# Kernel tuning notes

Measured on AMD Instinct MI355X. Metric: run time of the kernel, lower is better.

## Reference

```python
import jax, jax.numpy as jnp
import numpy as np

N = 50000
E = 1600000
EPS = 1e-16


def transformer_conv(x, src, dst, ea, Wq, bq, Wk, bk, Wv, bv, We, Ws, bs):
    # PyG TransformerConv, heads=1, concat=True, root_weight=True
    C = Wq.shape[1]
    q = x @ Wq + bq                      # [N, C]
    k = x @ Wk + bk                      # [N, C]
    v = x @ Wv + bv                      # [N, C]
    e = ea @ We                          # [E, C]
    k_e = k[src] + e                     # per-edge key
    v_e = v[src] + e                     # per-edge value
    score = (q[dst] * k_e).sum(-1) / jnp.sqrt(jnp.asarray(C, x.dtype))  # [E]
    # segment softmax over incoming edges of each dst node
    m = jax.ops.segment_max(score, dst, num_segments=N)
    ex = jnp.exp(score - m[dst])
    denom = jax.ops.segment_sum(ex, dst, num_segments=N)
    alpha = ex / (denom[dst] + EPS)
    out = jax.ops.segment_sum(alpha[:, None] * v_e, dst, num_segments=N)
    return out + x @ Ws + bs             # skip connection


def gcn_conv(x, src, dst, W, b):
    # PyG GCNConv: self-loops + symmetric deg^-1/2 normalization
    n_idx = jnp.arange(N)
    src2 = jnp.concatenate([src, n_idx])
    dst2 = jnp.concatenate([dst, n_idx])
    deg = jax.ops.segment_sum(jnp.ones(E + N, x.dtype), dst2, num_segments=N)
    dinv = jnp.where(deg > 0, jax.lax.rsqrt(deg), 0.0)
    norm = dinv[src2] * dinv[dst2]       # [E+N]
    h = x @ W                            # [N, out]
    out = jax.ops.segment_sum(norm[:, None] * h[src2], dst2, num_segments=N)
    return out + b


def setup_inputs() -> dict:
    key = jax.random.key(0)
    ks = jax.random.split(key, 32)
    d = {}
    d['x'] = jax.random.normal(ks[0], (N, 128), jnp.float32)
    d['edge_index'] = jax.random.randint(ks[1], (2, E), 0, N, jnp.int64)
    d['edge_attr'] = jax.random.normal(ks[2], (E, 16), jnp.float32)
    shapes = dict(
        Wq1=(128, 96), bq1=(96,), Wk1=(128, 96), bk1=(96,), Wv1=(128, 96), bv1=(96,),
        We1=(16, 96), Ws1=(128, 96), bs1=(96,),
        Wq2=(96, 64), bq2=(64,), Wk2=(96, 64), bk2=(64,), Wv2=(96, 64), bv2=(64,),
        We2=(16, 64), Ws2=(96, 64), bs2=(64,),
        Wmu=(64, 32), bmu=(32,), Wls=(64, 32), bls=(32,))
    for i, (name, shp) in enumerate(shapes.items()):
        scale = 1.0 / np.sqrt(shp[0]) if len(shp) == 2 else 0.02
        d[name] = jax.random.normal(ks[3 + i], shp, jnp.float32) * scale
    return d


def reference(x, edge_index, edge_attr,
              Wq1, bq1, Wk1, bk1, Wv1, bv1, We1, Ws1, bs1,
              Wq2, bq2, Wk2, bk2, Wv2, bv2, We2, Ws2, bs2,
              Wmu, bmu, Wls, bls):
    src, dst = edge_index[0], edge_index[1]
    h = jax.nn.relu(transformer_conv(x, src, dst, edge_attr,
                                     Wq1, bq1, Wk1, bk1, Wv1, bv1, We1, Ws1, bs1))
    h = jax.nn.relu(transformer_conv(h, src, dst, edge_attr,
                                     Wq2, bq2, Wk2, bk2, Wv2, bv2, We2, Ws2, bs2))
    mu = gcn_conv(h, src, dst, Wmu, bmu)
    logstd = gcn_conv(h, src, dst, Wls, bls)
    return mu, logstd
```

## Files before the change

### kernel.cpp

```cpp
#include <hip/hip_runtime.h>
#include <math.h>


#define TPB 256
typedef unsigned int uint32;
typedef unsigned short u16;
typedef __attribute__((ext_vector_type(4))) float f32x4;
typedef __attribute__((ext_vector_type(4))) uint32 u32x4;
typedef __attribute__((ext_vector_type(8))) short bf16x8;

__device__ __forceinline__ uint32 f2bf(float f) {
    uint32 u = __float_as_uint(f);
    return (u + 0x7fffu + ((u >> 16) & 1u)) >> 16;
}
__device__ __forceinline__ float bf2f(uint32 b) { return __uint_as_float(b << 16); }

__global__ void hist_kernel(const int* __restrict__ dst, int* __restrict__ deg, int E) {
    int i = blockIdx.x * TPB + threadIdx.x;
    if (i < E) atomicAdd(&deg[__builtin_nontemporal_load(dst + i)], 1);
}

__global__ __launch_bounds__(1024) void scan1_kernel(const int* __restrict__ deg,
                                                     int* __restrict__ prowp,
                                                     int* __restrict__ bsum, int n) {
    __shared__ int wsum[16];
    __shared__ int woff[16];
    int tid = threadIdx.x;
    int i = blockIdx.x * 1024 + tid;
    int lane = tid & 63, w = tid >> 6;
    int dg = (i < n) ? deg[i] : 0;
    int x = (dg + 7) & ~7;
    int v = x;
#pragma unroll
    for (int off = 1; off < 64; off <<= 1) {
        int t = __shfl_up(v, off, 64);
        if (lane >= off) v += t;
    }
    if (lane == 63) wsum[w] = v;
    __syncthreads();
    if (tid < 64) {
        int s = (tid < 16) ? wsum[tid] : 0;
#pragma unroll
        for (int off = 1; off < 16; off <<= 1) {
            int t = __shfl_up(s, off, 64);
            if (lane >= off) s += t;
        }
        if (tid < 16) woff[tid] = s;
    }
    __syncthreads();
    int incl = v + (w ? woff[w - 1] : 0);
    if (i < n) prowp[i] = incl;
    if (tid == 1023) bsum[blockIdx.x] = incl;
}

__global__ void scan2_kernel(const int* __restrict__ bsum, int* __restrict__ boff,
                             int* __restrict__ prowpN, int nb) {
    int tid = threadIdx.x;
    int x = (tid < nb) ? bsum[tid] : 0;
    int v = x;
#pragma unroll
    for (int off = 1; off < 64; off <<= 1) {
        int t = __shfl_up(v, off, 64);
        if (tid >= off) v += t;
    }
    if (tid < nb) boff[tid] = v - x;
    if (tid == nb - 1) *prowpN = v;
}

__global__ __launch_bounds__(1024) void scan3_kernel(const int* __restrict__ deg,
                                                     const int* __restrict__ boff,
                                                     int* __restrict__ prowp,
                                                     int* __restrict__ cursor,
                                                     float* __restrict__ dinv, int n) {
    int i = blockIdx.x * 1024 + threadIdx.x;
    if (i < n) {
        int dg = deg[i];
        int x = (dg + 7) & ~7;
        int excl = prowp[i] - x + boff[blockIdx.x];
        prowp[i] = excl;
        cursor[i] = excl;
        dinv[i] = 1.0f / sqrtf((float)(dg + 1));
    }
}

__global__ void scatter_kernel(const int* __restrict__ src, const int* __restrict__ dst,
                               const float* __restrict__ EA,
                               int* __restrict__ cursor,
                               int* __restrict__ psrc, u16* __restrict__ EAb, int E) {
    int i = blockIdx.x * TPB + threadIdx.x;
    if (i >= E) return;
    int pos = atomicAdd(&cursor[__builtin_nontemporal_load(dst + i)], 1);
    psrc[pos] = __builtin_nontemporal_load(src + i);
    const f32x4* e4 = (const f32x4*)(EA + (size_t)i * 16);
    f32x4 a = __builtin_nontemporal_load(e4);
    f32x4 b = __builtin_nontemporal_load(e4 + 1);
    f32x4 c = __builtin_nontemporal_load(e4 + 2);
    f32x4 d = __builtin_nontemporal_load(e4 + 3);
    u32x4* o = (u32x4*)(EAb + (size_t)pos * 16);
    u32x4 lo = {f2bf(a.x) | (f2bf(a.y) << 16), f2bf(a.z) | (f2bf(a.w) << 16),
                f2bf(b.x) | (f2bf(b.y) << 16), f2bf(b.z) | (f2bf(b.w) << 16)};
    u32x4 hi = {f2bf(c.x) | (f2bf(c.y) << 16), f2bf(c.z) | (f2bf(c.w) << 16),
                f2bf(d.x) | (f2bf(d.y) << 16), f2bf(d.z) | (f2bf(d.w) << 16)};
    o[0] = lo;
    o[1] = hi;
}

__global__ void padfill_kernel(const int* __restrict__ prowp, const int* __restrict__ deg,
                               int* __restrict__ psrc, u16* __restrict__ EAb, int N) {
    int n = blockIdx.x * TPB + threadIdx.x;
    if (n >= N) return;
    int p = prowp[n] + deg[n], pe = prowp[n + 1];
    u32x4 z = {0u, 0u, 0u, 0u};
    for (; p < pe; ++p) {
        psrc[p] = N;
        u32x4* o = (u32x4*)(EAb + (size_t)p * 16);
        o[0] = z;
        o[1] = z;
    }
}

__global__ void pack_kernel(
    const float* Wq1, const float* Wk1, const float* Wv1, const float* Ws1,
    const float* bq1, const float* bk1, const float* bv1, const float* bs1,
    const float* We1,
    const float* Wq2, const float* Wk2, const float* Wv2, const float* Ws2,
    const float* bq2, const float* bk2, const float* bv2, const float* bs2,
    const float* We2,
    const float* Wmu, const float* bmu, const float* Wls, const float* bls,
    const float* x, unsigned short* xb, int NX,
    unsigned short* Wc1t, float* bc1, unsigned short* Wc2t, float* bc2,
    float* Wc3, float* bc3) {
    const float s1 = 0.1020620726159658f;
    const float s2 = 0.125f;
    int gi = blockIdx.x * TPB + threadIdx.x;
    const int R0 = 448 * 128, R1 = R0 + 320 * 96, R2 = R1 + 64 * 64;
    const int R3 = R2 + 448, R4 = R3 + 320, R5 = R4 + 64;
    for (int i = gi; i < R5; i += gridDim.x * TPB) {
        if (i < R0) {
            int c = i / 128, kk = i % 128;
            float v = 0.f;
            if (c < 96) v = Wq1[kk * 96 + c] * s1;
            else if (c < 112) {
                int t = c - 96; float a = 0.f;
                for (int u = 0; u < 96; ++u) a += Wq1[kk * 96 + u] * We1[t * 96 + u];
                v = a * s1;
            } else if (c < 304) {
                int tt = c - 112;
                v = (tt & 1) ? Wv1[kk * 96 + (tt >> 1)] : Wk1[kk * 96 + (tt >> 1)];
            } else if (c < 400) v = Ws1[kk * 96 + (c - 304)];
            Wc1t[i] = (unsigned short)f2bf(v);
        } else if (i < R1) {
            int j = i - R0;
            int c = j / 96, kk = j % 96;
            float v = 0.f;
            if (c < 64) v = Wq2[kk * 64 + c] * s2;
            else if (c < 80) {
                int t = c - 64; float a = 0.f;
                for (int u = 0; u < 64; ++u) a += Wq2[kk * 64 + u] * We2[t * 64 + u];
                v = a * s2;
            } else if (c < 208) {
                int tt = c - 80;
                v = (tt & 1) ? Wv2[kk * 64 + (tt >> 1)] : Wk2[kk * 64 + (tt >> 1)];
            } else if (c < 272) v = Ws2[kk * 64 + (c - 208)];
            Wc2t[j] = (unsigned short)f2bf(v);
        } else if (i < R2) {
            int j = i - R1;
            int k = j / 64, c = j % 64;
            Wc3[j] = (c < 32) ? Wmu[k * 32 + c] : Wls[k * 32 + (c - 32)];
        } else if (i < R3) {
            int c = i - R2;
            float v = 0.f;
            if (c < 96) v = bq1[c] * s1;
            else if (c < 112) {
                int t = c - 96; float a = 0.f;
                for (int u = 0; u < 96; ++u) a += bq1[u] * We1[t * 96 + u];
                v = a * s1;
            } else if (c < 304) {
                int tt = c - 112;
                v = (tt & 1) ? bv1[tt >> 1] : bk1[tt >> 1];
            } else if (c < 400) v = bs1[c - 304];
            bc1[c] = v;
        } else if (i < R4) {
            int c = i - R3;
            float v = 0.f;
            if (c < 64) v = bq2[c] * s2;
            else if (c < 80) {
                int t = c - 64; float a = 0.f;
                for (int u = 0; u < 64; ++u) a += bq2[u] * We2[t * 64 + u];
                v = a * s2;
            } else if (c < 208) {
                int tt = c - 80;
                v = (tt & 1) ? bv2[tt >> 1] : bk2[tt >> 1];
            } else if (c < 272) v = bs2[c - 208];
            bc2[c] = v;
        } else {
            int c = i - R4;
            bc3[c] = (c < 32) ? bmu[c] : bls[c - 32];
        }
    }
    for (int i = gi; i < NX; i += gridDim.x * TPB)
        xb[i] = (unsigned short)f2bf(x[i]);
}

__global__ __launch_bounds__(256) void mfma_gemm_kernel(
    const unsigned short* __restrict__ A,
    const unsigned short* __restrict__ Wt,
    const float* __restrict__ bias,
    float* __restrict__ Qs, float* __restrict__ QE,
    uint32* __restrict__ KVp, float* __restrict__ SK,
    int N, int K, int Cq) {
    __shared__ unsigned short As[64][56];
    __shared__ unsigned short Bs[64][56];
    int r0 = blockIdx.x * 64, c0 = blockIdx.y * 64;
    int tid = threadIdx.x;
    int lane = tid & 63, w = tid >> 6;
    int wm = w >> 1, wn = w & 1;
    int l15 = lane & 15, l4 = lane >> 4;
    f32x4 zero = {0.f, 0.f, 0.f, 0.f};
    f32x4 acc[2][2] = {{zero, zero}, {zero, zero}};
    int sr = tid >> 2, sk = (tid & 3) * 8;

    for (int kc = 0; kc < K; kc += 32) {
        bf16x8 av = {};
        int ar = r0 + sr;
        if (ar < N) av = *(const bf16x8*)(A + (size_t)ar * K + kc + sk);
        *(bf16x8*)&As[sr][sk] = av;
        bf16x8 bv = *(const bf16x8*)(Wt + (size_t)(c0 + sr) * K + kc + sk);
        *(bf16x8*)&Bs[sr][sk] = bv;
        __syncthreads();
        bf16x8 af0 = *(const bf16x8*)&As[32 * wm + l15][l4 * 8];
        bf16x8 af1 = *(const bf16x8*)&As[32 * wm + 16 + l15][l4 * 8];
        bf16x8 bf0 = *(const bf16x8*)&Bs[32 * wn + l15][l4 * 8];
        bf16x8 bf1 = *(const bf16x8*)&Bs[32 * wn + 16 + l15][l4 * 8];
        acc[0][0] = __builtin_amdgcn_mfma_f32_16x16x32_bf16(af0, bf0, acc[0][0], 0, 0, 0);
        acc[0][1] = __builtin_amdgcn_mfma_f32_16x16x32_bf16(af0, bf1, acc[0][1], 0, 0, 0);
        acc[1][0] = __builtin_amdgcn_mfma_f32_16x16x32_bf16(af1, bf0, acc[1][0], 0, 0, 0);
        acc[1][1] = __builtin_amdgcn_mfma_f32_16x16x32_bf16(af1, bf1, acc[1][1], 0, 0, 0);
        __syncthreads();
    }

    int qe0 = Cq, kv0 = Cq + 16, sk0 = 3 * Cq + 16, end0 = 4 * Cq + 16;
#pragma unroll
    for (int fm = 0; fm < 2; ++fm) {
#pragma unroll
        for (int fn = 0; fn < 2; ++fn) {
            int cb = c0 + 32 * wn + 16 * fn;
            int c = cb + l15;
            float bia = bias[c];
#pragma unroll
            for (int r = 0; r < 4; ++r) {
                int row = r0 + 32 * wm + 16 * fm + l4 * 4 + r;
                float v = acc[fm][fn][r] + bia;
                float pv = __shfl_xor(v, 1, 64);
                bool ok = row < N;
                if (cb < qe0) {
                    if (ok) Qs[(size_t)row * Cq + c] = v;
                } else if (cb < kv0) {
                    if (ok) QE[(size_t)row * 16 + (c - qe0)] = v;
                } else if (cb < sk0) {
                    if (ok && !(l15 & 1)) {
                        int t = c - kv0;
                        KVp[(size_t)row * Cq + (t >> 1)] = (f2bf(v) << 16) | f2bf(pv);
                    }
                } else if (cb < end0) {
                    if (ok) SK[(size_t)row * Cq + (c - sk0)] = v;
                }
            }
        }
    }
}

template <int C>
__global__ __launch_bounds__(256) void edge_attn_kernel(
    const float* __restrict__ Qs, const float* __restrict__ SK,
    const uint32* __restrict__ KVp,
    const u16* __restrict__ EAb, const float* __restrict__ QE,
    const int* __restrict__ prowp, const int* __restrict__ deg,
    const int* __restrict__ psrc,
    float* __restrict__ Hpre, float* __restrict__ AEA, int N) {
    constexpr int CPL = C / 32;
    int n = blockIdx.x * 4 + (threadIdx.x >> 6);
    if (n >= N) return;
    int lane = threadIdx.x & 63;
    int half = lane >> 5, l = lane & 31, t16 = l & 15;
    bool lo16 = (l < 16);

    uint32 nC = (uint32)n * C;
    float q[CPL], acc[CPL];
#pragma unroll
    for (int j = 0; j < CPL; ++j) { q[j] = Qs[nC + l + 32 * j]; acc[j] = 0.f; }
    float qe = lo16 ? QE[(uint32)n * 16 + t16] : 0.f;
    float d = 0.f, aea = 0.f;
    int eb = prowp[n], ee = prowp[n + 1];

    for (int base = eb + 8 * half; base < ee; base += 16) {
        const int* sp = psrc + base;
        const u16* ep = EAb + (size_t)base * 16 + t16;
        float dots[8], eav[8];
        uint32 kv[8][CPL];
#pragma unroll
        for (int u = 0; u < 8; ++u) {
            int s = __builtin_nontemporal_load(sp + u);
            eav[u] = bf2f(__builtin_nontemporal_load(ep + u * 16));
            uint32 off = (uint32)s * C + l;
            float dt = qe * eav[u];
#pragma unroll
            for (int j = 0; j < CPL; ++j) {
                uint32 t = KVp[off + 32 * j];
                kv[u][j] = t;
                dt = fmaf(q[j], __uint_as_float(t & 0xffff0000u), dt);
            }
            dots[u] = dt;
        }
#pragma unroll
        for (int a = 0; a < 4; ++a) {
            float x0 = dots[2 * a], x1 = dots[2 * a + 1];
            float z = (lo16 ? x0 : x1) + __shfl_xor(lo16 ? x1 : x0, 16, 64);
            z += __shfl_xor(z, 8, 64);
            z += __shfl_xor(z, 4, 64);
            z += __shfl_xor(z, 2, 64);
            z += __shfl_xor(z, 1, 64);
            float p = __expf(z);
            float p0 = __shfl(p, 0, 32);
            float p1 = __shfl(p, 16, 32);
            d += p0 + p1;
            aea = fmaf(p0, eav[2 * a], fmaf(p1, eav[2 * a + 1], aea));
#pragma unroll
            for (int j = 0; j < CPL; ++j)
                acc[j] = fmaf(p0, __uint_as_float(kv[2 * a][j] << 16),
                         fmaf(p1, __uint_as_float(kv[2 * a + 1][j] << 16), acc[j]));
        }
    }
    d += __shfl_xor(d, 32, 64);
    aea += __shfl_xor(aea, 32, 64);
    d -= (float)((ee - eb) - deg[n]);
    float inv = 1.f / (d + 1e-16f);
#pragma unroll
    for (int j = 0; j < CPL; ++j) {
        float a2 = acc[j] + __shfl_xor(acc[j], 32, 64);
        if (half == 0)
            Hpre[nC + l + 32 * j] = a2 * inv + SK[nC + l + 32 * j];
    }
    if (lane < 16) AEA[(uint32)n * 16 + t16] = aea * inv;
}

template <int C>
__global__ void fixup_relu_kernel(const float* __restrict__ Hpre, const float* __restrict__ AEA,
                                  const float* __restrict__ We,
                                  unsigned short* __restrict__ H1b, int NC) {
    int idx = blockIdx.x * TPB + threadIdx.x;
    if (idx >= NC) return;
    int n = idx / C, c = idx % C;
    const float* a = AEA + (size_t)n * 16;
    float s = Hpre[idx];
#pragma unroll
    for (int t = 0; t < 16; ++t) s += a[t] * We[t * C + c];
    H1b[idx] = (unsigned short)f2bf(fmaxf(s, 0.f));
}

__global__ void fixup2_kernel(const float* __restrict__ Hpre, const float* __restrict__ AEA,
                              const float* __restrict__ We, const float* __restrict__ dinv,
                              uint32* __restrict__ H2p, int N) {
    int idx = blockIdx.x * TPB + threadIdx.x;
    if (idx >= N * 32) return;
    int n = idx >> 5, c = idx & 31;
    const float* a = AEA + (size_t)n * 16;
    float s0 = Hpre[(size_t)n * 64 + c];
    float s1 = Hpre[(size_t)n * 64 + 32 + c];
#pragma unroll
    for (int t = 0; t < 16; ++t) {
        s0 += a[t] * We[t * 64 + c];
        s1 += a[t] * We[t * 64 + 32 + c];
    }
    float dn = dinv[n];
    s0 = fmaxf(s0, 0.f) * dn;
    s1 = fmaxf(s1, 0.f) * dn;
    H2p[idx] = f2bf(s0) | (f2bf(s1) << 16);
}

__global__ __launch_bounds__(256) void gcn_agg_kernel(
    const uint32* __restrict__ H2p, const int* __restrict__ prowp,
    const int* __restrict__ psrc, const float* __restrict__ dinv,
    float* __restrict__ AGG, int N) {
    int n = blockIdx.x * 4 + (threadIdx.x >> 6);
    if (n >= N) return;
    int lane = threadIdx.x & 63, half = lane >> 5, l = lane & 31;
    float s0 = 0.f, s1 = 0.f;
    int eb = prowp[n], ee = prowp[n + 1];
    for (int base = eb + 8 * half; base < ee; base += 16) {
        const int* sp = psrc + base;
#pragma unroll
        for (int u = 0; u < 8; ++u) {
            int s = __builtin_nontemporal_load(sp + u);
            uint32 t = H2p[(uint32)s * 32 + l];
            s0 += bf2f(t & 0xffffu);
            s1 += __uint_as_float(t & 0xffff0000u);
        }
    }
    s0 += __shfl_xor(s0, 32, 64);
    s1 += __shfl_xor(s1, 32, 64);
    if (half == 0) {
        uint32 u = H2p[(uint32)n * 32 + l];
        float dn = dinv[n];
        AGG[(uint32)n * 64 + l]      = dn * (s0 + bf2f(u & 0xffffu));
        AGG[(uint32)n * 64 + 32 + l] = dn * (s1 + __uint_as_float(u & 0xffff0000u));
    }
}

template <int CT, bool SPLIT>
__global__ __launch_bounds__(256) void gemm_kernel(
    const float* __restrict__ A, const float* __restrict__ W,
    const float* __restrict__ bias, float* __restrict__ Out,
    float* __restrict__ Out2, int N, int K, int C) {
    constexpr int TC = CT / 16;
    __shared__ float As[32][68];
    __shared__ float Bs[32][CT + 4];
    int r0 = blockIdx.x * 64, c0 = blockIdx.y * CT;
    int t = threadIdx.x;
    int tr = t >> 4, tc = t & 15;
    float acc[4][TC];
#pragma unroll
    for (int i = 0; i < 4; ++i)
#pragma unroll
        for (int j = 0; j < TC; ++j) acc[i][j] = 0.f;

    for (int kc = 0; kc < K; kc += 32) {
        int ra = t >> 2, kq = (t & 3) * 8;
        float4 a0 = {0, 0, 0, 0}, a1 = {0, 0, 0, 0};
        int r = r0 + ra;
        if (r < N) {
            const float* ap = A + (size_t)r * K + kc + kq;
            a0 = *(const float4*)ap;
            a1 = *(const float4*)(ap + 4);
        }
        As[kq + 0][ra] = a0.x; As[kq + 1][ra] = a0.y;
        As[kq + 2][ra] = a0.z; As[kq + 3][ra] = a0.w;
        As[kq + 4][ra] = a1.x; As[kq + 5][ra] = a1.y;
        As[kq + 6][ra] = a1.z; As[kq + 7][ra] = a1.w;
        constexpr int PASSES = (32 * CT) / (256 * 8);
#pragma unroll
        for (int p = 0; p < PASSES; ++p) {
            int idx = (t + p * 256) * 8;
            int k = idx / CT, c = idx % CT;
            const float* wp = W + (size_t)(kc + k) * C + c0 + c;
            float4 b0 = *(const float4*)wp;
            float4 b1 = *(const float4*)(wp + 4);
            *(float4*)&Bs[k][c] = b0;
            *(float4*)&Bs[k][c + 4] = b1;
        }
        __syncthreads();
#pragma unroll
        for (int k = 0; k < 32; ++k) {
            float4 av = *(const float4*)&As[k][tr * 4];
            float a[4] = {av.x, av.y, av.z, av.w};
#pragma unroll
            for (int u = 0; u < TC / 4; ++u) {
                float4 bv = *(const float4*)&Bs[k][tc * TC + u * 4];
                float b[4] = {bv.x, bv.y, bv.z, bv.w};
#pragma unroll
                for (int i = 0; i < 4; ++i)
#pragma unroll
                    for (int j = 0; j < 4; ++j) acc[i][u * 4 + j] += a[i] * b[j];
            }
        }
        __syncthreads();
    }
#pragma unroll
    for (int i = 0; i < 4; ++i) {
        int r = r0 + tr * 4 + i;
        if (r >= N) continue;
#pragma unroll
        for (int j = 0; j < TC; ++j) {
            int c = c0 + tc * TC + j;
            float v = acc[i][j] + bias[c];
            if (SPLIT) {
                if (c < 32) Out[(size_t)r * 32 + c] = v;
                else        Out2[(size_t)r * 32 + c - 32] = v;
            } else {
                Out[(size_t)r * C + c] = v;
            }
        }
    }
}

extern "C" void kernel_launch(void* const* d_in, const int* in_sizes, int n_in,
                              void* d_out, int out_size, void* d_ws, size_t ws_size,
                              hipStream_t stream) {
    const float* x   = (const float*)d_in[0];
    const int*   ei  = (const int*)d_in[1];
    const float* ea  = (const float*)d_in[2];
    const float* Wq1 = (const float*)d_in[3];  const float* bq1 = (const float*)d_in[4];
    const float* Wk1 = (const float*)d_in[5];  const float* bk1 = (const float*)d_in[6];
    const float* Wv1 = (const float*)d_in[7];  const float* bv1 = (const float*)d_in[8];
    const float* We1 = (const float*)d_in[9];
    const float* Ws1 = (const float*)d_in[10]; const float* bs1 = (const float*)d_in[11];
    const float* Wq2 = (const float*)d_in[12]; const float* bq2 = (const float*)d_in[13];
    const float* Wk2 = (const float*)d_in[14]; const float* bk2 = (const float*)d_in[15];
    const float* Wv2 = (const float*)d_in[16]; const float* bv2 = (const float*)d_in[17];
    const float* We2 = (const float*)d_in[18];
    const float* Ws2 = (const float*)d_in[19]; const float* bs2 = (const float*)d_in[20];
    const float* Wmu = (const float*)d_in[21]; const float* bmu = (const float*)d_in[22];
    const float* Wls = (const float*)d_in[23]; const float* bls = (const float*)d_in[24];

    int N = in_sizes[0] / 128;
    int E = in_sizes[1] / 2;
    const int* src = ei;
    const int* dst = ei + E;
    int E2max = E + 8 * N;

    char* ws = (char*)d_ws;
    size_t off = 0;
    auto alloc = [&](size_t bytes) -> char* {
        char* p = ws + off;
        off = (off + bytes + 255) & ~(size_t)255;
        return p;
    };
    int*      deg    = (int*)alloc((size_t)N * 4);
    int*      prowp  = (int*)alloc((size_t)(N + 1) * 4);
    int*      cursor = (int*)alloc((size_t)N * 4);
    float*    dinv   = (float*)alloc((size_t)N * 4);
    int*      bsum   = (int*)alloc(256 * 4);
    int*      boff   = (int*)alloc(256 * 4);
    int*      psrc   = (int*)alloc((size_t)E2max * 4);
    u16*      EAb    = (u16*)alloc((size_t)E2max * 16 * 2);
    unsigned short* Wc1t = (unsigned short*)alloc(448 * 128 * 2);
    float*    bc1    = (float*)alloc(448 * 4);
    unsigned short* Wc2t = (unsigned short*)alloc(320 * 96 * 2);
    float*    bc2    = (float*)alloc(320 * 4);
    float*    Wc3    = (float*)alloc(64 * 64 * 4);
    float*    bc3    = (float*)alloc(64 * 4);
    unsigned short* xb = (unsigned short*)alloc((size_t)N * 128 * 2);
    float*    Qs   = (float*)alloc((size_t)N * 96 * 4);
    float*    QE   = (float*)alloc((size_t)N * 16 * 4);
    uint32*   KVp  = (uint32*)alloc((size_t)(N + 1) * 96 * 4);
    float*    SKb  = (float*)alloc((size_t)N * 96 * 4);
    float*    Hpre = (float*)alloc((size_t)N * 96 * 4);
    unsigned short* H1b = (unsigned short*)alloc((size_t)N * 96 * 2);
    float*    AEA  = (float*)alloc((size_t)N * 16 * 4);
    uint32*   H2p  = (uint32*)alloc((size_t)(N + 1) * 32 * 4);
    float*    AGG  = (float*)alloc((size_t)N * 64 * 4);

    (void)hipMemsetAsync(deg, 0, (size_t)N * 4, stream);
    (void)hipMemsetAsync(KVp + (size_t)N * 96, 0, 96 * 4, stream);
    (void)hipMemsetAsync(H2p + (size_t)N * 32, 0, 32 * 4, stream);

    int ebk = (E + TPB - 1) / TPB;
    int nb1k = (N + 1023) / 1024;
    int nbN = (N + TPB - 1) / TPB;
    hist_kernel<<<ebk, TPB, 0, stream>>>(dst, deg, E);
    scan1_kernel<<<nb1k, 1024, 0, stream>>>(deg, prowp, bsum, N);
    scan2_kernel<<<1, 64, 0, stream>>>(bsum, boff, prowp + N, nb1k);
    scan3_kernel<<<nb1k, 1024, 0, stream>>>(deg, boff, prowp, cursor, dinv, N);
    scatter_kernel<<<ebk, TPB, 0, stream>>>(src, dst, ea, cursor, psrc, EAb, E);
    padfill_kernel<<<nbN, TPB, 0, stream>>>(prowp, deg, psrc, EAb, N);
    pack_kernel<<<364, TPB, 0, stream>>>(Wq1, Wk1, Wv1, Ws1, bq1, bk1, bv1, bs1, We1,
                                         Wq2, Wk2, Wv2, Ws2, bq2, bk2, bv2, bs2, We2,
                                         Wmu, bmu, Wls, bls, x, xb, N * 128,
                                         Wc1t, bc1, Wc2t, bc2, Wc3, bc3);

    int rb = (N + 63) / 64;
    int nb4 = (N + 3) / 4;

    mfma_gemm_kernel<<<dim3(rb, 7), 256, 0, stream>>>(xb, Wc1t, bc1, Qs, QE, KVp, SKb,
                                                      N, 128, 96);
    edge_attn_kernel<96><<<nb4, 256, 0, stream>>>(Qs, SKb, KVp, EAb, QE, prowp, deg, psrc,
                                                  Hpre, AEA, N);
    fixup_relu_kernel<96><<<(N * 96 + TPB - 1) / TPB, TPB, 0, stream>>>(Hpre, AEA, We1,
                                                                        H1b, N * 96);
    mfma_gemm_kernel<<<dim3(rb, 5), 256, 0, stream>>>(H1b, Wc2t, bc2, Qs, QE, KVp, SKb,
                                                      N, 96, 64);
    (void)hipMemsetAsync(KVp + (size_t)N * 64, 0, 64 * 4, stream);
    edge_attn_kernel<64><<<nb4, 256, 0, stream>>>(Qs, SKb, KVp, EAb, QE, prowp, deg, psrc,
                                                  Hpre, AEA, N);
    fixup2_kernel<<<(N * 32 + TPB - 1) / TPB, TPB, 0, stream>>>(Hpre, AEA, We2, dinv, H2p, N);
    gcn_agg_kernel<<<nb4, 256, 0, stream>>>(H2p, prowp, psrc, dinv, AGG, N);
    gemm_kernel<64, true><<<dim3(rb, 1), 256, 0, stream>>>(AGG, Wc3, bc3, (float*)d_out,
                                                           (float*)d_out + (size_t)N * 32,
                                                           N, 64, 64);
}
```

Baseline: 518.6 us.

## Store edge attributes in original order and index them via packed edge IDs

The scatter kernel now writes bf16 edge attributes sequentially by original edge index with nontemporal stores, instead of scattering 32-byte rows to CSR positions. The CSR array becomes a packed 64-bit (edge id, source) pair, and padding points at a zero row appended after the last edge. This makes the scatter pass write coalesced, but the edge-attention kernels now gather edge-attribute rows randomly through the edge id, and the CSR array read by three kernels doubles in size.

```diff
diff --git a/kernel.cpp b/kernel.cpp
--- a/kernel.cpp
+++ b/kernel.cpp
@@ -4,6 +4,7 @@
 
 #define TPB 256
 typedef unsigned int uint32;
+typedef unsigned long long u64;
 typedef unsigned short u16;
 typedef __attribute__((ext_vector_type(4))) float f32x4;
 typedef __attribute__((ext_vector_type(4))) uint32 u32x4;
@@ -86,37 +87,38 @@
 __global__ void scatter_kernel(const int* __restrict__ src, const int* __restrict__ dst,
                                const float* __restrict__ EA,
                                int* __restrict__ cursor,
-                               int* __restrict__ psrc, u16* __restrict__ EAb, int E) {
+                               u64* __restrict__ pse, u16* __restrict__ EAbE, int E) {
     int i = blockIdx.x * TPB + threadIdx.x;
     if (i >= E) return;
-    int pos = atomicAdd(&cursor[__builtin_nontemporal_load(dst + i)], 1);
-    psrc[pos] = __builtin_nontemporal_load(src + i);
+    int s = __builtin_nontemporal_load(src + i);
+    int d0 = __builtin_nontemporal_load(dst + i);
+    int pos = atomicAdd(&cursor[d0], 1);
+    pse[pos] = ((u64)(uint32)i << 32) | (uint32)s;
     const f32x4* e4 = (const f32x4*)(EA + (size_t)i * 16);
     f32x4 a = __builtin_nontemporal_load(e4);
     f32x4 b = __builtin_nontemporal_load(e4 + 1);
     f32x4 c = __builtin_nontemporal_load(e4 + 2);
     f32x4 d = __builtin_nontemporal_load(e4 + 3);
-    u32x4* o = (u32x4*)(EAb + (size_t)pos * 16);
     u32x4 lo = {f2bf(a.x) | (f2bf(a.y) << 16), f2bf(a.z) | (f2bf(a.w) << 16),
                 f2bf(b.x) | (f2bf(b.y) << 16), f2bf(b.z) | (f2bf(b.w) << 16)};
     u32x4 hi = {f2bf(c.x) | (f2bf(c.y) << 16), f2bf(c.z) | (f2bf(c.w) << 16),
                 f2bf(d.x) | (f2bf(d.y) << 16), f2bf(d.z) | (f2bf(d.w) << 16)};
-    o[0] = lo;
-    o[1] = hi;
+    u32x4* o = (u32x4*)(EAbE + (size_t)i * 16);
+    __builtin_nontemporal_store(lo, o);
+    __builtin_nontemporal_store(hi, o + 1);
 }
 
 __global__ void padfill_kernel(const int* __restrict__ prowp, const int* __restrict__ deg,
-                               int* __restrict__ psrc, u16* __restrict__ EAb, int N) {
+                               u64* __restrict__ pse, int N, int E) {
     int n = blockIdx.x * TPB + threadIdx.x;
     if (n >= N) return;
     int p = prowp[n] + deg[n], pe = prowp[n + 1];
-    u32x4 z = {0u, 0u, 0u, 0u};
-    for (; p < pe; ++p) {
-        psrc[p] = N;
-        u32x4* o = (u32x4*)(EAb + (size_t)p * 16);
-        o[0] = z;
-        o[1] = z;
-    }
+    u64 pad = ((u64)(uint32)E << 32) | (uint32)N;
+    for (; p < pe; ++p) pse[p] = pad;
+}
+
+__global__ void zerorow_kernel(u16* __restrict__ EAbE, int E) {
+    if (threadIdx.x < 16) EAbE[(size_t)E * 16 + threadIdx.x] = 0;
 }
 
 __global__ void pack_kernel(
@@ -274,9 +276,9 @@
 __global__ __launch_bounds__(256) void edge_attn_kernel(
     const float* __restrict__ Qs, const float* __restrict__ SK,
     const uint32* __restrict__ KVp,
-    const u16* __restrict__ EAb, const float* __restrict__ QE,
+    const u16* __restrict__ EAbE, const float* __restrict__ QE,
     const int* __restrict__ prowp, const int* __restrict__ deg,
-    const int* __restrict__ psrc,
+    const u64* __restrict__ pse,
     float* __restrict__ Hpre, float* __restrict__ AEA, int N) {
     constexpr int CPL = C / 32;
     int n = blockIdx.x * 4 + (threadIdx.x >> 6);
@@ -294,15 +296,16 @@
     int eb = prowp[n], ee = prowp[n + 1];
 
     for (int base = eb + 8 * half; base < ee; base += 16) {
-        const int* sp = psrc + base;
-        const u16* ep = EAb + (size_t)base * 16 + t16;
+        const u64* pp = pse + base;
         float dots[8], eav[8];
         uint32 kv[8][CPL];
 #pragma unroll
         for (int u = 0; u < 8; ++u) {
-            int s = __builtin_nontemporal_load(sp + u);
-            eav[u] = bf2f(__builtin_nontemporal_load(ep + u * 16));
-            uint32 off = (uint32)s * C + l;
+            u64 pk = __builtin_nontemporal_load(pp + u);
+            uint32 s = (uint32)pk;
+            uint32 eid = (uint32)(pk >> 32);
+            eav[u] = bf2f((uint32)EAbE[(size_t)eid * 16 + t16]);
+            uint32 off = s * C + l;
             float dt = qe * eav[u];
 #pragma unroll
             for (int j = 0; j < CPL; ++j) {
@@ -380,7 +383,7 @@
 
 __global__ __launch_bounds__(256) void gcn_agg_kernel(
     const uint32* __restrict__ H2p, const int* __restrict__ prowp,
-    const int* __restrict__ psrc, const float* __restrict__ dinv,
+    const u64* __restrict__ pse, const float* __restrict__ dinv,
     float* __restrict__ AGG, int N) {
     int n = blockIdx.x * 4 + (threadIdx.x >> 6);
     if (n >= N) return;
@@ -388,11 +391,11 @@
     float s0 = 0.f, s1 = 0.f;
     int eb = prowp[n], ee = prowp[n + 1];
     for (int base = eb + 8 * half; base < ee; base += 16) {
-        const int* sp = psrc + base;
+        const u64* pp = pse + base;
 #pragma unroll
         for (int u = 0; u < 8; ++u) {
-            int s = __builtin_nontemporal_load(sp + u);
-            uint32 t = H2p[(uint32)s * 32 + l];
+            uint32 s = (uint32)__builtin_nontemporal_load(pp + u);
+            uint32 t = H2p[s * 32 + l];
             s0 += bf2f(t & 0xffffu);
             s1 += __uint_as_float(t & 0xffff0000u);
         }
@@ -521,8 +524,8 @@
     float*    dinv   = (float*)alloc((size_t)N * 4);
     int*      bsum   = (int*)alloc(256 * 4);
     int*      boff   = (int*)alloc(256 * 4);
-    int*      psrc   = (int*)alloc((size_t)E2max * 4);
-    u16*      EAb    = (u16*)alloc((size_t)E2max * 16 * 2);
+    u64*      pse    = (u64*)alloc((size_t)E2max * 8);
+    u16*      EAbE   = (u16*)alloc((size_t)(E + 1) * 16 * 2);
     unsigned short* Wc1t = (unsigned short*)alloc(448 * 128 * 2);
     float*    bc1    = (float*)alloc(448 * 4);
     unsigned short* Wc2t = (unsigned short*)alloc(320 * 96 * 2);
@@ -551,8 +554,9 @@
     scan1_kernel<<<nb1k, 1024, 0, stream>>>(deg, prowp, bsum, N);
     scan2_kernel<<<1, 64, 0, stream>>>(bsum, boff, prowp + N, nb1k);
     scan3_kernel<<<nb1k, 1024, 0, stream>>>(deg, boff, prowp, cursor, dinv, N);
-    scatter_kernel<<<ebk, TPB, 0, stream>>>(src, dst, ea, cursor, psrc, EAb, E);
-    padfill_kernel<<<nbN, TPB, 0, stream>>>(prowp, deg, psrc, EAb, N);
+    scatter_kernel<<<ebk, TPB, 0, stream>>>(src, dst, ea, cursor, pse, EAbE, E);
+    padfill_kernel<<<nbN, TPB, 0, stream>>>(prowp, deg, pse, N, E);
+    zerorow_kernel<<<1, 64, 0, stream>>>(EAbE, E);
     pack_kernel<<<364, TPB, 0, stream>>>(Wq1, Wk1, Wv1, Ws1, bq1, bk1, bv1, bs1, We1,
                                          Wq2, Wk2, Wv2, Ws2, bq2, bk2, bv2, bs2, We2,
                                          Wmu, bmu, Wls, bls, x, xb, N * 128,
@@ -563,17 +567,17 @@
 
     mfma_gemm_kernel<<<dim3(rb, 7), 256, 0, stream>>>(xb, Wc1t, bc1, Qs, QE, KVp, SKb,
                                                       N, 128, 96);
-    edge_attn_kernel<96><<<nb4, 256, 0, stream>>>(Qs, SKb, KVp, EAb, QE, prowp, deg, psrc,
+    edge_attn_kernel<96><<<nb4, 256, 0, stream>>>(Qs, SKb, KVp, EAbE, QE, prowp, deg, pse,
                                                   Hpre, AEA, N);
     fixup_relu_kernel<96><<<(N * 96 + TPB - 1) / TPB, TPB, 0, stream>>>(Hpre, AEA, We1,
                                                                         H1b, N * 96);
     mfma_gemm_kernel<<<dim3(rb, 5), 256, 0, stream>>>(H1b, Wc2t, bc2, Qs, QE, KVp, SKb,
                                                       N, 96, 64);
     (void)hipMemsetAsync(KVp + (size_t)N * 64, 0, 64 * 4, stream);
-    edge_attn_kernel<64><<<nb4, 256, 0, stream>>>(Qs, SKb, KVp, EAb, QE, prowp, deg, psrc,
+    edge_attn_kernel<64><<<nb4, 256, 0, stream>>>(Qs, SKb, KVp, EAbE, QE, prowp, deg, pse,
                                                   Hpre, AEA, N);
     fixup2_kernel<<<(N * 32 + TPB - 1) / TPB, TPB, 0, stream>>>(Hpre, AEA, We2, dinv, H2p, N);
-    gcn_agg_kernel<<<nb4, 256, 0, stream>>>(H2p, prowp, psrc, dinv, AGG, N);
+    gcn_agg_kernel<<<nb4, 256, 0, stream>>>(H2p, prowp, pse, dinv, AGG, N);
     gemm_kernel<64, true><<<dim3(rb, 1), 256, 0, stream>>>(AGG, Wc3, bc3, (float*)d_out,
                                                            (float*)d_out + (size_t)N * 32,
                                                            N, 64, 64);
```

Measured after the change: 536.2 us. +3.4%, slower.

## Scatter packed (edge id, src) pairs, then permute edge attributes with coalesced writes

Applied to the files above, without the earlier changes.

The scatter kernel no longer writes 32-byte bf16 edge-attribute rows to random CSR positions. It writes one 64-bit (edge id, src) word per edge. A new permute kernel then walks CSR positions in order, gathers the fp32 edge attributes by edge id, and writes psrc and EAb with coalesced nontemporal stores. Padding slots are filled in scan3, so the padfill kernel is gone. The trade is an extra pass and an 8-byte-per-edge buffer in exchange for sequential writes instead of scattered ones.

```diff
diff --git a/kernel.cpp b/kernel.cpp
--- a/kernel.cpp
+++ b/kernel.cpp
@@ -4,6 +4,7 @@
 
 #define TPB 256
 typedef unsigned int uint32;
+typedef unsigned long long u64;
 typedef unsigned short u16;
 typedef __attribute__((ext_vector_type(4))) float f32x4;
 typedef __attribute__((ext_vector_type(4))) uint32 u32x4;
@@ -71,7 +72,8 @@
                                                      const int* __restrict__ boff,
                                                      int* __restrict__ prowp,
                                                      int* __restrict__ cursor,
-                                                     float* __restrict__ dinv, int n) {
+                                                     float* __restrict__ dinv,
+                                                     u64* __restrict__ pse, int n) {
     int i = blockIdx.x * 1024 + threadIdx.x;
     if (i < n) {
         int dg = deg[i];
@@ -80,43 +82,48 @@
         prowp[i] = excl;
         cursor[i] = excl;
         dinv[i] = 1.0f / sqrtf((float)(dg + 1));
+        u64 pad = (u64)(uint32)n;
+        for (int p = excl + dg; p < excl + x; ++p) pse[p] = pad;
     }
 }
 
 __global__ void scatter_kernel(const int* __restrict__ src, const int* __restrict__ dst,
-                               const float* __restrict__ EA,
-                               int* __restrict__ cursor,
-                               int* __restrict__ psrc, u16* __restrict__ EAb, int E) {
+                               int* __restrict__ cursor, u64* __restrict__ pse, int E) {
     int i = blockIdx.x * TPB + threadIdx.x;
     if (i >= E) return;
-    int pos = atomicAdd(&cursor[__builtin_nontemporal_load(dst + i)], 1);
-    psrc[pos] = __builtin_nontemporal_load(src + i);
-    const f32x4* e4 = (const f32x4*)(EA + (size_t)i * 16);
-    f32x4 a = __builtin_nontemporal_load(e4);
-    f32x4 b = __builtin_nontemporal_load(e4 + 1);
-    f32x4 c = __builtin_nontemporal_load(e4 + 2);
-    f32x4 d = __builtin_nontemporal_load(e4 + 3);
-    u32x4* o = (u32x4*)(EAb + (size_t)pos * 16);
-    u32x4 lo = {f2bf(a.x) | (f2bf(a.y) << 16), f2bf(a.z) | (f2bf(a.w) << 16),
-                f2bf(b.x) | (f2bf(b.y) << 16), f2bf(b.z) | (f2bf(b.w) << 16)};
-    u32x4 hi = {f2bf(c.x) | (f2bf(c.y) << 16), f2bf(c.z) | (f2bf(c.w) << 16),
-                f2bf(d.x) | (f2bf(d.y) << 16), f2bf(d.z) | (f2bf(d.w) << 16)};
-    o[0] = lo;
-    o[1] = hi;
-}
-
-__global__ void padfill_kernel(const int* __restrict__ prowp, const int* __restrict__ deg,
-                               int* __restrict__ psrc, u16* __restrict__ EAb, int N) {
-    int n = blockIdx.x * TPB + threadIdx.x;
-    if (n >= N) return;
-    int p = prowp[n] + deg[n], pe = prowp[n + 1];
-    u32x4 z = {0u, 0u, 0u, 0u};
-    for (; p < pe; ++p) {
-        psrc[p] = N;
-        u32x4* o = (u32x4*)(EAb + (size_t)p * 16);
-        o[0] = z;
-        o[1] = z;
-    }
+    int s = __builtin_nontemporal_load(src + i);
+    int d0 = __builtin_nontemporal_load(dst + i);
+    int pos = atomicAdd(&cursor[d0], 1);
+    pse[pos] = ((u64)(uint32)i << 32) | (uint32)s;
+}
+
+__global__ void permute_kernel(const u64* __restrict__ pse, const float* __restrict__ EA,
+                               const int* __restrict__ prowpN,
+                               int* __restrict__ psrc, u16* __restrict__ EAb,
+                               int N, int cap) {
+    int i = blockIdx.x * TPB + threadIdx.x;
+    if (i >= cap) return;
+    int tot = *prowpN;
+    if (i >= tot) return;
+    u64 pk = __builtin_nontemporal_load(pse + i);
+    uint32 s = (uint32)pk;
+    uint32 eid = (uint32)(pk >> 32);
+    __builtin_nontemporal_store((int)s, psrc + i);
+    u32x4 lo = {0u, 0u, 0u, 0u}, hi = {0u, 0u, 0u, 0u};
+    if (s != (uint32)N) {
+        const f32x4* e4 = (const f32x4*)(EA + (size_t)eid * 16);
+        f32x4 a = __builtin_nontemporal_load(e4);
+        f32x4 b = __builtin_nontemporal_load(e4 + 1);
+        f32x4 c = __builtin_nontemporal_load(e4 + 2);
+        f32x4 d = __builtin_nontemporal_load(e4 + 3);
+        lo = (u32x4){f2bf(a.x) | (f2bf(a.y) << 16), f2bf(a.z) | (f2bf(a.w) << 16),
+                     f2bf(b.x) | (f2bf(b.y) << 16), f2bf(b.z) | (f2bf(b.w) << 16)};
+        hi = (u32x4){f2bf(c.x) | (f2bf(c.y) << 16), f2bf(c.z) | (f2bf(c.w) << 16),
+                     f2bf(d.x) | (f2bf(d.y) << 16), f2bf(d.z) | (f2bf(d.w) << 16)};
+    }
+    u32x4* o = (u32x4*)(EAb + (size_t)i * 16);
+    __builtin_nontemporal_store(lo, o);
+    __builtin_nontemporal_store(hi, o + 1);
 }
 
 __global__ void pack_kernel(
@@ -391,8 +398,8 @@
         const int* sp = psrc + base;
 #pragma unroll
         for (int u = 0; u < 8; ++u) {
-            int s = __builtin_nontemporal_load(sp + u);
-            uint32 t = H2p[(uint32)s * 32 + l];
+            uint32 s = (uint32)__builtin_nontemporal_load(sp + u);
+            uint32 t = H2p[s * 32 + l];
             s0 += bf2f(t & 0xffffu);
             s1 += __uint_as_float(t & 0xffff0000u);
         }
@@ -521,6 +528,7 @@
     float*    dinv   = (float*)alloc((size_t)N * 4);
     int*      bsum   = (int*)alloc(256 * 4);
     int*      boff   = (int*)alloc(256 * 4);
+    u64*      pse    = (u64*)alloc((size_t)E2max * 8);
     int*      psrc   = (int*)alloc((size_t)E2max * 4);
     u16*      EAb    = (u16*)alloc((size_t)E2max * 16 * 2);
     unsigned short* Wc1t = (unsigned short*)alloc(448 * 128 * 2);
@@ -545,14 +553,14 @@
     (void)hipMemsetAsync(H2p + (size_t)N * 32, 0, 32 * 4, stream);
 
     int ebk = (E + TPB - 1) / TPB;
+    int e2bk = (E2max + TPB - 1) / TPB;
     int nb1k = (N + 1023) / 1024;
-    int nbN = (N + TPB - 1) / TPB;
     hist_kernel<<<ebk, TPB, 0, stream>>>(dst, deg, E);
     scan1_kernel<<<nb1k, 1024, 0, stream>>>(deg, prowp, bsum, N);
     scan2_kernel<<<1, 64, 0, stream>>>(bsum, boff, prowp + N, nb1k);
-    scan3_kernel<<<nb1k, 1024, 0, stream>>>(deg, boff, prowp, cursor, dinv, N);
-    scatter_kernel<<<ebk, TPB, 0, stream>>>(src, dst, ea, cursor, psrc, EAb, E);
-    padfill_kernel<<<nbN, TPB, 0, stream>>>(prowp, deg, psrc, EAb, N);
+    scan3_kernel<<<nb1k, 1024, 0, stream>>>(deg, boff, prowp, cursor, dinv, pse, N);
+    scatter_kernel<<<ebk, TPB, 0, stream>>>(src, dst, cursor, pse, E);
+    permute_kernel<<<e2bk, TPB, 0, stream>>>(pse, ea, prowp + N, psrc, EAb, N, E2max);
     pack_kernel<<<364, TPB, 0, stream>>>(Wq1, Wk1, Wv1, Ws1, bq1, bk1, bv1, bs1, We1,
                                          Wq2, Wk2, Wv2, Ws2, bq2, bk2, bv2, bs2, We2,
                                          Wmu, bmu, Wls, bls, x, xb, N * 128,
```

After: 619.4 us. 19.4% more time.
